# Performance work log

Measured on AMD Instinct MI355X. Metric: run time of the kernel, lower is better.

Reference implementation:

```python
import jax, jax.numpy as jnp
import numpy as np

RENDER_SIZE = 256   # renderer image_size
IMG_H, IMG_W = 480, 640
ORIG_SIZE = 640     # max(H, W)
SIGMA = 0.5         # soft-silhouette sharpness in pixels (approximates NR hard rasterizer)
CHUNK = 128         # faces per scan step (bounds peak memory)
N_VERTS = 2048
N_FACES = 4096


def _se3_exp(dof):
    """dof = [v(3), omega(3)] (pytorch3d order) -> (R [3,3], t [3]) column convention."""
    v, w = dof[:3], dof[3:]
    th2 = jnp.sum(w * w)
    th = jnp.sqrt(th2 + 1e-30)
    small = th < 1e-4
    th_s = jnp.where(small, 1.0, th)          # safe denom (avoids nan grads)
    th2_s = jnp.where(small, 1.0, th2)
    A = jnp.where(small, 1.0 - th2 / 6.0, jnp.sin(th_s) / th_s)
    B = jnp.where(small, 0.5 - th2 / 24.0, (1.0 - jnp.cos(th_s)) / th2_s)
    C = jnp.where(small, 1.0 / 6.0 - th2 / 120.0, (th_s - jnp.sin(th_s)) / (th2_s * th_s))
    Kx = jnp.array([[0.0, -w[2], w[1]], [w[2], 0.0, -w[0]], [-w[1], w[0], 0.0]], dtype=dof.dtype)
    K2 = Kx @ Kx
    I = jnp.eye(3, dtype=dof.dtype)
    R = I + A * Kx + B * K2
    V = I + B * Kx + C * K2   # left Jacobian
    return R, V @ v


def _cross2(u, w):
    return u[..., 0] * w[..., 1] - u[..., 1] * w[..., 0]


def _rasterize_silhouette(tri):
    """tri: [F,3,2] projected triangle verts in render-pixel coords -> [R,R] coverage."""
    P = RENDER_SIZE * RENDER_SIZE
    ys, xs = jnp.meshgrid(jnp.arange(RENDER_SIZE, dtype=jnp.float32) + 0.5,
                          jnp.arange(RENDER_SIZE, dtype=jnp.float32) + 0.5, indexing='ij')
    px, py = xs.reshape(-1), ys.reshape(-1)  # [P] pixel centers
    tris = tri.reshape(N_FACES // CHUNK, CHUNK, 3, 2)

    def body(logp, t3):
        a = t3                          # [C,3,2] edge start verts
        e = jnp.roll(t3, -1, axis=1) - a  # [C,3,2] edge vectors (v1-v0, v2-v1, v0-v2)
        area2 = _cross2(e[:, 0], -e[:, 2])            # signed doubled area, [C]
        sgn = jnp.where(area2 >= 0, 1.0, -1.0)        # winding fix so inside > 0
        elen = jnp.sqrt(jnp.sum(e * e, -1)) + 1e-9    # [C,3]
        c0 = e[..., 0] * a[..., 1] - e[..., 1] * a[..., 0]  # [C,3]
        # signed distance of each pixel to each edge line: [P,C,3]
        d = (e[None, :, :, 0] * py[:, None, None] - e[None, :, :, 1] * px[:, None, None] - c0[None]) / elen[None]
        d = sgn[None, :, None] * d
        dmin = jnp.min(d, axis=2)                     # [P,C] min edge distance
        s = jnp.minimum(jax.nn.sigmoid(dmin / SIGMA), 1.0 - 1e-6)
        return logp + jnp.sum(jnp.log1p(-s), axis=1), None

    logp, _ = jax.lax.scan(body, jnp.zeros(P, jnp.float32), tris)
    return (1.0 - jnp.exp(logp)).reshape(RENDER_SIZE, RENDER_SIZE)


def _resize_nearest(img, size):
    return jax.image.resize(img, (size, size), method='nearest')


def reference(dof, vertices, faces, K, mask_gt):
    R, t = _se3_exp(dof)
    cam = vertices @ R.T + t              # [N,3] camera coords
    uvw = cam @ K.T                       # pinhole projection
    xy = uvw[:, :2] / uvw[:, 2:3]         # pixel coords at orig_size resolution
    xy = xy * (RENDER_SIZE / ORIG_SIZE)   # scale to render grid
    tri = xy[faces]                       # [F,3,2]
    si = _rasterize_silhouette(tri)       # [R,R]
    si = _resize_nearest(si, ORIG_SIZE)[:IMG_H, :IMG_W]
    loss = jnp.sum((si - mask_gt) ** 2)
    return loss, si


def setup_inputs() -> dict:
    key = jax.random.key(0)
    k1, k2, k3, k4 = jax.random.split(key, 4)
    v = jax.random.normal(k1, (N_VERTS, 3), dtype=jnp.float32)
    vertices = 0.5 * v / (jnp.linalg.norm(v, axis=1, keepdims=True) + 1e-8)  # unit-ish sphere mesh
    faces = jax.random.randint(k2, (N_FACES, 3), 0, N_VERTS, dtype=jnp.int32)
    # pose: object ~2.5m in front of camera, small rotation + noise
    dof = jnp.array([0.0, 0.0, 2.5, 0.2, -0.1, 0.15], dtype=jnp.float32) \
          + 0.05 * jax.random.normal(k3, (6,), dtype=jnp.float32)
    K = jnp.array([[600.0, 0.0, 320.0], [0.0, 600.0, 240.0], [0.0, 0.0, 1.0]], dtype=jnp.float32)
    mask_gt = (jax.random.uniform(k4, (IMG_H, IMG_W)) < 0.3).astype(jnp.float32)
    return {"dof": dof, "vertices": vertices, "faces": faces, "K": K, "mask_gt": mask_gt}
```

## Files before the change

### kernel.cpp

```cpp
#include <hip/hip_runtime.h>
#include <math.h>

#define RENDER 256
#define IMG_H 480
#define IMG_W 640
#define NV 2048
#define NF 4096
#define FACE_SLICES 16
#define FACES_PER_SLICE (NF / FACE_SLICES)
#define TILES 256
#define N_UNITS (TILES * FACE_SLICES)

#define SIGMA_INV 2.0f
#define CAP 13.815510557964274f
#define LOG2E 1.4426950408889634f
#define ZK 2.8853900817779268f
#define CAP2 19.931568569324174f
#define THR_CAP2  50.8f
#define THR_SKIP2 -56.6f

#define WS_FD_OFF    0
#define WS_LOGP_OFF  (192 * 1024)

__global__ __launch_bounds__(256) void k_prep(const float* __restrict__ dof,
                                              const float* __restrict__ verts,
                                              const int* __restrict__ faces,
                                              const float* __restrict__ Km,
                                              float* __restrict__ fdata,
                                              float* __restrict__ logp,
                                              float* __restrict__ out) {
    if (blockIdx.x >= 16) {
        logp[(blockIdx.x - 16) * 256 + threadIdx.x] = 0.0f;
        if (blockIdx.x == 16 && threadIdx.x == 0) out[0] = 0.0f;
        return;
    }

    __shared__ float sxy[NV * 2];

    float v0 = dof[0], v1 = dof[1], v2 = dof[2];
    float w0 = dof[3], w1 = dof[4], w2 = dof[5];
    float th2 = w0 * w0 + w1 * w1 + w2 * w2;
    float th = sqrtf(th2 + 1e-30f);
    bool small = th < 1e-4f;
    float th_s = small ? 1.0f : th;
    float th2_s = small ? 1.0f : th2;
    float A = small ? (1.0f - th2 / 6.0f) : (sinf(th_s) / th_s);
    float B = small ? (0.5f - th2 / 24.0f) : ((1.0f - cosf(th_s)) / th2_s);
    float C = small ? (1.0f / 6.0f - th2 / 120.0f)
                    : ((th_s - sinf(th_s)) / (th2_s * th_s));
    float Kx[9] = {0.0f, -w2, w1, w2, 0.0f, -w0, -w1, w0, 0.0f};
    float w[3] = {w0, w1, w2};
    float R[9], V[9];
    for (int i = 0; i < 3; i++)
        for (int j = 0; j < 3; j++) {
            float K2 = w[i] * w[j] - (i == j ? th2 : 0.0f);
            float id = (i == j) ? 1.0f : 0.0f;
            R[i * 3 + j] = id + A * Kx[i * 3 + j] + B * K2;
            V[i * 3 + j] = id + B * Kx[i * 3 + j] + C * K2;
        }
    float t0 = V[0] * v0 + V[1] * v1 + V[2] * v2;
    float t1 = V[3] * v0 + V[4] * v1 + V[5] * v2;
    float t2 = V[6] * v0 + V[7] * v1 + V[8] * v2;
    float K00 = Km[0], K01 = Km[1], K02 = Km[2];
    float K10 = Km[3], K11 = Km[4], K12 = Km[5];
    float K20 = Km[6], K21 = Km[7], K22 = Km[8];
    const float scale = 256.0f / 640.0f;

    for (int n = threadIdx.x; n < NV; n += 256) {
        float vx = verts[n * 3], vy = verts[n * 3 + 1], vz = verts[n * 3 + 2];
        float cx = R[0] * vx + R[1] * vy + R[2] * vz + t0;
        float cy = R[3] * vx + R[4] * vy + R[5] * vz + t1;
        float cz = R[6] * vx + R[7] * vy + R[8] * vz + t2;
        float u = K00 * cx + K01 * cy + K02 * cz;
        float v = K10 * cx + K11 * cy + K12 * cz;
        float ww = K20 * cx + K21 * cy + K22 * cz;
        float rw = __builtin_amdgcn_rcpf(ww) * scale;
        sxy[n * 2]     = u * rw;
        sxy[n * 2 + 1] = v * rw;
    }
    __syncthreads();

    int f = blockIdx.x * 256 + threadIdx.x;
    int i0 = faces[f * 3], i1 = faces[f * 3 + 1], i2 = faces[f * 3 + 2];
    float x0 = sxy[i0 * 2], y0 = sxy[i0 * 2 + 1];
    float x1 = sxy[i1 * 2], y1 = sxy[i1 * 2 + 1];
    float x2 = sxy[i2 * 2], y2 = sxy[i2 * 2 + 1];
    float ex[3] = {x1 - x0, x2 - x1, x0 - x2};
    float ey[3] = {y1 - y0, y2 - y1, y0 - y2};
    float ax[3] = {x0, x1, x2};
    float ay[3] = {y0, y1, y2};
    float area2 = ex[0] * (-ey[2]) - ey[0] * (-ex[2]);
    float sgn = (area2 >= 0.0f) ? 1.0f : -1.0f;
    float* o = fdata + f * 12;
    for (int k = 0; k < 3; k++) {
        float elen = sqrtf(ex[k] * ex[k] + ey[k] * ey[k]) + 1e-9f;
        float c0 = ex[k] * ay[k] - ey[k] * ax[k];
        float inv = sgn / elen * ZK;
        o[k * 4 + 0] = ex[k] * inv;
        o[k * 4 + 1] = -ey[k] * inv;
        o[k * 4 + 2] = -c0 * inv;
        o[k * 4 + 3] = 0.0f;
    }
}

__global__ __launch_bounds__(256) void k_raster(const float* __restrict__ fdata,
                                                float* __restrict__ logp) {
    __shared__ float s_data[4096];
    __shared__ int s_n;
    __shared__ int s_ncap;
    const int tid = threadIdx.x;
    if (tid == 0) { s_n = 0; s_ncap = 0; }
    __syncthreads();

    const int unit = (blockIdx.x * 2053) & (N_UNITS - 1);
    const int tile = unit >> 4;
    const int slice = unit & 15;
    const int tileX = tile & 15;
    const int tileY = tile >> 4;
    const float cx = tileX * 16 + 8.0f;
    const float cy = tileY * 16 + 8.0f;
    const float4* __restrict__ fd4 = (const float4*)fdata;

    {
        int f = slice * FACES_PER_SLICE + tid;
        float4 e0 = fd4[f * 3 + 0];
        float4 e1 = fd4[f * 3 + 1];
        float4 e2 = fd4[f * 3 + 2];
        float d0 = fmaf(e0.y, cx, fmaf(e0.x, cy, e0.z));
        float d1 = fmaf(e1.y, cx, fmaf(e1.x, cy, e1.z));
        float d2 = fmaf(e2.y, cx, fmaf(e2.x, cy, e2.z));
        float dmin = fminf(d0, fminf(d1, d2));
        bool capped = dmin > THR_CAP2;
        bool live = (!capped) && (dmin > THR_SKIP2);
        unsigned long long mcap = __ballot(capped);
        unsigned long long mliv = __ballot(live);
        int lane = tid & 63;
        int base = 0;
        if (lane == 0) {
            base = atomicAdd(&s_n, __popcll(mliv));
            atomicAdd(&s_ncap, __popcll(mcap));
        }
        base = __shfl(base, 0, 64);
        if (live) {
            int pos = base + __popcll(mliv & ((1ull << lane) - 1ull));
            float4* dst = (float4*)(s_data + pos * 12);
            dst[0] = e0; dst[1] = e1; dst[2] = e2;
        }
    }
    __syncthreads();

    const int n = s_n;
    const int ncap = s_ncap;
    if (n == 0 && ncap == 0) return;

    const int wv = tid >> 6;
    const int lane = tid & 63;
    const int row = lane >> 2;
    const int col0 = lane & 3;
    const float py = (float)(tileY * 16 + row) + 0.5f;
    const float px0 = (float)(tileX * 16 + col0) + 0.5f;

    float acc[4] = {0.0f, 0.0f, 0.0f, 0.0f};
    const float4* sd = (const float4*)s_data;
    if (wv < n) {
        float4 c0 = sd[wv * 3 + 0], c1 = sd[wv * 3 + 1], c2 = sd[wv * 3 + 2];
        for (int i = wv; i < n; i += 4) {
            float4 n0 = sd[(i + 4) * 3 + 0];
            float4 n1 = sd[(i + 4) * 3 + 1];
            float4 n2 = sd[(i + 4) * 3 + 2];
            float t0p = fmaf(c0.x, py, c0.z);
            float t1p = fmaf(c1.x, py, c1.z);
            float t2p = fmaf(c2.x, py, c2.z);
            #pragma unroll
            for (int k = 0; k < 4; ++k) {
                float px = px0 + (float)(4 * k);
                float z = fminf(fmaf(c0.y, px, t0p),
                          fminf(fmaf(c1.y, px, t1p), fmaf(c2.y, px, t2p)));
                float e = __builtin_amdgcn_exp2f(z);
                float sp2 = __builtin_amdgcn_logf(1.0f + e);
                acc[k] -= fminf(sp2, CAP2);
            }
            c0 = n0; c1 = n1; c2 = n2;
        }
    }

    __syncthreads();
    {
        int base = wv * 1024 + row * 16 + col0;
        s_data[base + 0]  = acc[0];
        s_data[base + 4]  = acc[1];
        s_data[base + 8]  = acc[2];
        s_data[base + 12] = acc[3];
    }
    __syncthreads();
    {
        int p = tid;
        float v = s_data[p] + s_data[1024 + p] + s_data[2048 + p] +
                  s_data[3072 + p] - CAP2 * (float)ncap;
        int iyp = tileY * 16 + (p >> 4);
        int ixp = tileX * 16 + (p & 15);
        atomicAdd(&logp[iyp * RENDER + ixp], v);
    }
}

__global__ __launch_bounds__(256) void k_final(const float* __restrict__ logp,
                                               const float* __restrict__ mask,
                                               float* __restrict__ out) {
    int idx = blockIdx.x * 256 + threadIdx.x;
    int r = idx / IMG_W;
    int c = idx - r * IMG_W;
    int ir = (2 * r + 1) / 5;
    int ic = (2 * c + 1) / 5;
    float si = 1.0f - __builtin_amdgcn_exp2f(logp[ir * RENDER + ic]);
    out[1 + idx] = si;
    float diff = si - mask[idx];
    float d2 = diff * diff;
    #pragma unroll
    for (int off = 32; off > 0; off >>= 1) d2 += __shfl_down(d2, off, 64);
    __shared__ float sred[4];
    int lane = threadIdx.x & 63;
    int wv = threadIdx.x >> 6;
    if (lane == 0) sred[wv] = d2;
    __syncthreads();
    if (threadIdx.x == 0)
        atomicAdd(out, sred[0] + sred[1] + sred[2] + sred[3]);
}

extern "C" void kernel_launch(void* const* d_in, const int* in_sizes, int n_in,
                              void* d_out, int out_size, void* d_ws, size_t ws_size,
                              hipStream_t stream) {
    const float* dof   = (const float*)d_in[0];
    const float* verts = (const float*)d_in[1];
    const int*   faces = (const int*)d_in[2];
    const float* Km    = (const float*)d_in[3];
    const float* mask  = (const float*)d_in[4];
    float* out = (float*)d_out;

    char* ws = (char*)d_ws;
    float* fdata = (float*)(ws + WS_FD_OFF);
    float* logp  = (float*)(ws + WS_LOGP_OFF);

    k_prep<<<272, 256, 0, stream>>>(dof, verts, faces, Km, fdata, logp, out);
    k_raster<<<N_UNITS, 256, 0, stream>>>(fdata, logp);
    k_final<<<(IMG_H * IMG_W) / 256, 256, 0, stream>>>(logp, mask, out);
}
```

Before: 105.2 us.

## Replace per-face log with running product and tighten per-tile cull bounds

```diff
diff --git a/kernel.cpp b/kernel.cpp
--- a/kernel.cpp
+++ b/kernel.cpp
@@ -16,8 +16,8 @@
 #define LOG2E 1.4426950408889634f
 #define ZK 2.8853900817779268f
 #define CAP2 19.931568569324174f
-#define THR_CAP2  50.8f
-#define THR_SKIP2 -56.6f
+#define ECAP 999999.0f
+#define SKIP_PIX -26.0f
 
 #define WS_FD_OFF    0
 #define WS_LOGP_OFF  (192 * 1024)
@@ -96,10 +96,12 @@
         float elen = sqrtf(ex[k] * ex[k] + ey[k] * ey[k]) + 1e-9f;
         float c0 = ex[k] * ay[k] - ey[k] * ax[k];
         float inv = sgn / elen * ZK;
-        o[k * 4 + 0] = ex[k] * inv;
-        o[k * 4 + 1] = -ey[k] * inv;
+        float Ac = ex[k] * inv;
+        float Bc = -ey[k] * inv;
+        o[k * 4 + 0] = Ac;
+        o[k * 4 + 1] = Bc;
         o[k * 4 + 2] = -c0 * inv;
-        o[k * 4 + 3] = 0.0f;
+        o[k * 4 + 3] = 7.5f * (fabsf(Ac) + fabsf(Bc));
     }
 }
 
@@ -129,9 +131,10 @@
         float d0 = fmaf(e0.y, cx, fmaf(e0.x, cy, e0.z));
         float d1 = fmaf(e1.y, cx, fmaf(e1.x, cy, e1.z));
         float d2 = fmaf(e2.y, cx, fmaf(e2.x, cy, e2.z));
-        float dmin = fminf(d0, fminf(d1, d2));
-        bool capped = dmin > THR_CAP2;
-        bool live = (!capped) && (dmin > THR_SKIP2);
+        float capm = fminf(d0 - e0.w, fminf(d1 - e1.w, d2 - e2.w));
+        float skpm = fminf(d0 + e0.w, fminf(d1 + e1.w, d2 + e2.w));
+        bool capped = capm > CAP2;
+        bool live = (!capped) && (skpm > SKIP_PIX);
         unsigned long long mcap = __ballot(capped);
         unsigned long long mliv = __ballot(live);
         int lane = tid & 63;
@@ -160,10 +163,12 @@
     const float py = (float)(tileY * 16 + row) + 0.5f;
     const float px0 = (float)(tileX * 16 + col0) + 0.5f;
 
-    float acc[4] = {0.0f, 0.0f, 0.0f, 0.0f};
+    float pm[4] = {1.0f, 1.0f, 1.0f, 1.0f};
+    int   pe[4] = {0, 0, 0, 0};
     const float4* sd = (const float4*)s_data;
     if (wv < n) {
         float4 c0 = sd[wv * 3 + 0], c1 = sd[wv * 3 + 1], c2 = sd[wv * 3 + 2];
+        int it = 0;
         for (int i = wv; i < n; i += 4) {
             float4 n0 = sd[(i + 4) * 3 + 0];
             float4 n1 = sd[(i + 4) * 3 + 1];
@@ -176,13 +181,24 @@
                 float px = px0 + (float)(4 * k);
                 float z = fminf(fmaf(c0.y, px, t0p),
                           fminf(fmaf(c1.y, px, t1p), fmaf(c2.y, px, t2p)));
-                float e = __builtin_amdgcn_exp2f(z);
-                float sp2 = __builtin_amdgcn_logf(1.0f + e);
-                acc[k] -= fminf(sp2, CAP2);
+                float e = fminf(__builtin_amdgcn_exp2f(z), ECAP);
+                pm[k] = fmaf(pm[k], e, pm[k]);
+            }
+            if (((++it) & 3) == 0) {
+                #pragma unroll
+                for (int k = 0; k < 4; ++k) {
+                    unsigned b = __float_as_uint(pm[k]);
+                    pe[k] += (int)(b >> 23) - 127;
+                    pm[k] = __uint_as_float((b & 0x007fffffu) | 0x3f800000u);
+                }
             }
             c0 = n0; c1 = n1; c2 = n2;
         }
     }
+    float acc[4];
+    #pragma unroll
+    for (int k = 0; k < 4; ++k)
+        acc[k] = -((float)pe[k] + __builtin_amdgcn_logf(pm[k]));
 
     __syncthreads();
     {
```

Measured after the change: 104.0 us. No clear change (-1.1%).
